# Performance work log

Hardware: AMD Instinct MI355X
Metric: run time of the kernel (lower is better)

Reference implementation:

```python
import jax, jax.numpy as jnp
import numpy as np

N = 100000   # nodes
E = 800000   # edges
F_IN = 16
H = 64       # hidden_dim
L = 4        # num_layers
CD = 8       # contrastive_dim
BN_EPS = 1e-5


def setup_inputs() -> dict:
    key = jax.random.key(0)
    ks = jax.random.split(key, 20)
    s = 0.05
    return {
        "x": jax.random.normal(ks[0], (N, F_IN), jnp.float32),
        "edge_index": jax.random.randint(ks[1], (2, E), 0, N, jnp.int64),
        "batch": jnp.zeros((N,), jnp.int64),
        "enc_w1": jax.random.normal(ks[2], (F_IN, H), jnp.float32) * s,
        "enc_b1": jnp.zeros((H,), jnp.float32),
        "enc_w2": jax.random.normal(ks[3], (H, H), jnp.float32) * s,
        "enc_b2": jnp.zeros((H,), jnp.float32),
        "conv_w": jax.random.normal(ks[4], (L, 2 * H, H), jnp.float32) * s,
        "conv_b": jnp.zeros((L, H), jnp.float32),
        "bn_gamma": jnp.ones((L, H), jnp.float32),
        "bn_beta": jnp.zeros((L, H), jnp.float32),
        "out_w1": jax.random.normal(ks[5], (H, 64), jnp.float32) * s,
        "out_b1": jnp.zeros((64,), jnp.float32),
        "out_w2": jax.random.normal(ks[6], (64, 32), jnp.float32) * s,
        "out_b2": jnp.zeros((32,), jnp.float32),
        "out_w3": jax.random.normal(ks[7], (32, CD), jnp.float32) * s,
        "out_b3": jnp.zeros((CD,), jnp.float32),
    }


def _forward(x, edge_index, enc_w1, enc_b1, enc_w2, enc_b2,
             conv_w, conv_b, bn_gamma, bn_beta,
             out_w1, out_b1, out_w2, out_b2, out_w3, out_b3):
    row, col = edge_index[0], edge_index[1]
    # lc_encode: Linear+ELU, Linear+ELU
    h = jax.nn.elu(x @ enc_w1 + enc_b1)
    feats = jax.nn.elu(h @ enc_w2 + enc_b2)  # (N, H)

    ones = jnp.ones((E, 1), feats.dtype)
    counts = jnp.clip(jax.ops.segment_sum(ones, row, num_segments=N), 1.0)  # (N,1)
    bn_scale = 1.0 / jnp.sqrt(1.0 + BN_EPS)  # eval-mode BN: running_mean=0, running_var=1

    for i in range(L):
        xc = feats[row]               # gather centers (E, H)
        xn = feats[col]               # gather neighbors (E, H)
        ef = jnp.concatenate([xc, xn - xc], axis=-1)      # (E, 2H)
        e = jax.nn.elu(ef @ conv_w[i] + conv_b[i])        # Linear + ELU
        e = (e * bn_scale) * bn_gamma[i] + bn_beta[i]     # BatchNorm (eval); Dropout is identity
        agg = jax.ops.segment_sum(e, row, num_segments=N) / counts
        feats = agg + feats  # residual in Net.forward

    # output head (Dropout identity in eval)
    o = jax.nn.elu(feats @ out_w1 + out_b1)
    o = jax.nn.elu(o @ out_w2 + out_b2)
    return o @ out_w3 + out_b3  # (N, CD)


def reference(x, edge_index, batch, enc_w1, enc_b1, enc_w2, enc_b2,
              conv_w, conv_b, bn_gamma, bn_beta,
              out_w1, out_b1, out_w2, out_b2, out_w3, out_b3):
    out = _forward(x, edge_index, enc_w1, enc_b1, enc_w2, enc_b2,
                   conv_w, conv_b, bn_gamma, bn_beta,
                   out_w1, out_b1, out_w2, out_b2, out_w3, out_b3)
    return (out, batch)
```

## Files before the change

### kernel.cpp

```cpp
#include <hip/hip_runtime.h>

#define NN 100000
#define NE 800000
#define FIN 16
#define H 64
#define NL 4
#define CDIM 8
#define NT 1563
#define NABF 1563
#define NGB 6250
#define NGF 12500
#define ROWS_PER_OWN 12500
#define ECHUNK 2048
#define NCHUNK ((NE + ECHUNK - 1) / ECHUNK)
#define NSC (NCHUNK * 8)
#define CAP 32
#define HOT 8
#define SPILL (CAP - HOT)

typedef __attribute__((ext_vector_type(8))) short bf16x8;
typedef __attribute__((ext_vector_type(4))) float f32x4;

__device__ __forceinline__ float elu(float x) { return x > 0.f ? x : __expf(x) - 1.f; }
__device__ __forceinline__ float4 elu4(float4 v) {
    return make_float4(elu(v.x), elu(v.y), elu(v.z), elu(v.w));
}

__device__ __forceinline__ unsigned short f2bf(float x) {
    union { float f; unsigned int u; } v; v.f = x;
    unsigned int r = v.u + 0x7fffu + ((v.u >> 16) & 1u);
    return (unsigned short)(r >> 16);
}
__device__ __forceinline__ float u2f(unsigned int u) {
    union { unsigned int u; float f; } v; v.u = u;
    return v.f;
}

__global__ __launch_bounds__(256) void k_enc(const float* __restrict__ x,
                                             const float* __restrict__ w1,
                                             const float* __restrict__ b1,
                                             const float* __restrict__ w2,
                                             const float* __restrict__ b2,
                                             float* __restrict__ feats,
                                             int* __restrict__ cnt,
                                             const float* __restrict__ convw,
                                             unsigned short* __restrict__ WT) {
    int tid = threadIdx.x;
    if (blockIdx.x >= NT) {
        int t = (blockIdx.x - NT) * 256 + tid;
        int i = t >> 11;
        int rem = t & 2047;
        int j = rem >> 4;
        int kg = rem & 15;
        const float* W = convw + (size_t)i * 2 * H * H;
        float v[4];
#pragma unroll
        for (int q = 0; q < 4; q++) {
            int k = kg * 4 + q;
            if (j < 64) v[q] = W[k * 64 + j] - W[(64 + k) * 64 + j];
            else        v[q] = W[(64 + k) * 64 + (j - 64)];
        }
        ushort4 p;
        p.x = f2bf(v[0]); p.y = f2bf(v[1]); p.z = f2bf(v[2]); p.w = f2bf(v[3]);
        *(ushort4*)&WT[(size_t)i * 8192 + j * 64 + kg * 4] = p;
        return;
    }
    __shared__ __align__(16) float xs[64 * 16];
    __shared__ __align__(16) float w1s[16 * 64];
    __shared__ __align__(16) float ws[64 * 64];
    __shared__ __align__(16) float fs[64 * 68];
    int base = blockIdx.x * 64;
    {
        int gid = blockIdx.x * 256 + tid;
        if (gid < NN) cnt[gid] = 0;
    }
    {
        size_t ei = (size_t)base * FIN + tid * 4;
        size_t emax = (size_t)NN * FIN - 4;
        if (ei > emax) ei = emax;
        *(float4*)&xs[tid * 4] = *(const float4*)&x[ei];
    }
    ((float4*)w1s)[tid] = ((const float4*)w1)[tid];
#pragma unroll
    for (int r = 0; r < 4; r++) ((float4*)ws)[tid + 256 * r] = ((const float4*)w2)[tid + 256 * r];
    __syncthreads();

    int wave = tid >> 6, j = tid & 63;
    float bb1 = b1[j];
    for (int i = 0; i < 16; i++) {
        int nl = i * 4 + wave;
        float acc = bb1;
#pragma unroll
        for (int k = 0; k < FIN; k++) acc += xs[nl * FIN + k] * w1s[k * 64 + j];
        fs[nl * 68 + j] = elu(acc);
    }
    __syncthreads();

    int cg = tid & 15, ng = tid >> 4;
    int c0 = cg * 4;
    float4 bb = ((const float4*)b2)[cg];
    float4 acc[4];
    acc[0] = bb; acc[1] = bb; acc[2] = bb; acc[3] = bb;
#pragma unroll 2
    for (int kq = 0; kq < 16; kq++) {
        int k0 = kq * 4;
        float4 w0 = *(const float4*)&ws[(k0 + 0) * 64 + c0];
        float4 w1v = *(const float4*)&ws[(k0 + 1) * 64 + c0];
        float4 w2v = *(const float4*)&ws[(k0 + 2) * 64 + c0];
        float4 w3v = *(const float4*)&ws[(k0 + 3) * 64 + c0];
#pragma unroll
        for (int m = 0; m < 4; m++) {
            float4 f = *(const float4*)&fs[(ng * 4 + m) * 68 + k0];
            acc[m].x += f.x * w0.x + f.y * w1v.x + f.z * w2v.x + f.w * w3v.x;
            acc[m].y += f.x * w0.y + f.y * w1v.y + f.z * w2v.y + f.w * w3v.y;
            acc[m].z += f.x * w0.z + f.y * w1v.z + f.z * w2v.z + f.w * w3v.z;
            acc[m].w += f.x * w0.w + f.y * w1v.w + f.z * w2v.w + f.w * w3v.w;
        }
    }
#pragma unroll
    for (int m = 0; m < 4; m++) {
        int n = base + ng * 4 + m;
        if (n < NN) *(float4*)&feats[(size_t)n * 64 + c0] = elu4(acc[m]);
    }
}

__global__ __launch_bounds__(256, 8) void k_scab(const int* __restrict__ row,
                                                 const int* __restrict__ col,
                                                 int* cnt, int* __restrict__ hot,
                                                 int* __restrict__ spill,
                                                 const float* __restrict__ feats,
                                                 const unsigned short* __restrict__ WT,
                                                 const float* __restrict__ convb,
                                                 unsigned short* __restrict__ Am,
                                                 unsigned short* __restrict__ Bm) {
    int tid = threadIdx.x;
    if (blockIdx.x < NSC) {
        int owner = blockIdx.x & 7;
        int chunk = blockIdx.x >> 3;
        int lo = owner * ROWS_PER_OWN, hi = lo + ROWS_PER_OWN;
        int base = chunk * ECHUNK;
        int end = base + ECHUNK; if (end > NE) end = NE;
        for (int e = base + tid; e < end; e += 256) {
            int r = row[e];
            if (r >= lo && r < hi) {
                int p = atomicAdd(&cnt[r], 1);
                if (p < HOT) hot[(size_t)r * HOT + p] = col[e];
                else if (p < CAP) spill[(size_t)r * SPILL + (p - HOT)] = col[e];
            }
        }
        return;
    }
    int bid = blockIdx.x - NSC;
    int wave = tid >> 6, lane = tid & 63;
    int lr = lane & 15, lk = lane >> 4;
    int nb = bid * 64 + wave * 16;
    int n = nb + lr;
    int nc = n < NN ? n : NN - 1;

    bf16x8 ff0, ff1;
    {
        float4 f0 = *(const float4*)&feats[(size_t)nc * 64 + lk * 8];
        float4 f1 = *(const float4*)&feats[(size_t)nc * 64 + lk * 8 + 4];
        float4 f2 = *(const float4*)&feats[(size_t)nc * 64 + 32 + lk * 8];
        float4 f3 = *(const float4*)&feats[(size_t)nc * 64 + 32 + lk * 8 + 4];
        ff0[0] = (short)f2bf(f0.x); ff0[1] = (short)f2bf(f0.y);
        ff0[2] = (short)f2bf(f0.z); ff0[3] = (short)f2bf(f0.w);
        ff0[4] = (short)f2bf(f1.x); ff0[5] = (short)f2bf(f1.y);
        ff0[6] = (short)f2bf(f1.z); ff0[7] = (short)f2bf(f1.w);
        ff1[0] = (short)f2bf(f2.x); ff1[1] = (short)f2bf(f2.y);
        ff1[2] = (short)f2bf(f2.z); ff1[3] = (short)f2bf(f2.w);
        ff1[4] = (short)f2bf(f3.x); ff1[5] = (short)f2bf(f3.y);
        ff1[6] = (short)f2bf(f3.z); ff1[7] = (short)f2bf(f3.w);
    }
#pragma unroll 1
    for (int ct = 0; ct < 8; ct++) {
        bf16x8 w0 = *(const bf16x8*)&WT[(ct * 16 + lr) * 64 + lk * 8];
        bf16x8 w1 = *(const bf16x8*)&WT[(ct * 16 + lr) * 64 + 32 + lk * 8];
        f32x4 acc;
        if (ct < 4) {
            float4 bq = *(const float4*)&convb[ct * 16 + lk * 4];
            acc[0] = bq.x; acc[1] = bq.y; acc[2] = bq.z; acc[3] = bq.w;
        } else {
            acc = (f32x4)(0.0f);
        }
        acc = __builtin_amdgcn_mfma_f32_16x16x32_bf16(w0, ff0, acc, 0, 0, 0);
        acc = __builtin_amdgcn_mfma_f32_16x16x32_bf16(w1, ff1, acc, 0, 0, 0);
        if (n < NN) {
            unsigned short* dst = (ct < 4) ? Am : Bm;
            int wc = (ct & 3) * 16 + lk * 4;
            ushort4 p;
            p.x = f2bf(acc[0]); p.y = f2bf(acc[1]);
            p.z = f2bf(acc[2]); p.w = f2bf(acc[3]);
            *(ushort4*)&dst[(size_t)n * 64 + wc] = p;
        }
    }
}

__global__ __launch_bounds__(256) void k_gab(const unsigned short* __restrict__ Brd,
                                             unsigned short* __restrict__ Am,
                                             unsigned short* __restrict__ Bwr,
                                             const int* __restrict__ cnt,
                                             const int* __restrict__ hot,
                                             const int* __restrict__ spill,
                                             const float* __restrict__ gamma,
                                             const float* __restrict__ beta,
                                             float* __restrict__ feats,
                                             const unsigned short* __restrict__ WT,
                                             const float* __restrict__ convb) {
    __shared__ __align__(16) unsigned short nlds[16 * 72];
    int tid = threadIdx.x;
    int wave = tid >> 6, lane = tid & 63;
    int half = lane >> 5, l = lane & 31;
    int g = l >> 3;
    int cq = l & 7, c0 = cq * 8;
    int nb16 = blockIdx.x * 16;

    const float bs = 0.99999500003749968750f;
    float4 gm0 = *(const float4*)&gamma[c0];
    float4 gm1 = *(const float4*)&gamma[c0 + 4];
    float4 bt0 = *(const float4*)&beta[c0];
    float4 bt1 = *(const float4*)&beta[c0 + 4];

#pragma unroll
    for (int t = 0; t < 2; t++) {
        int j = t * 8 + wave * 2 + half;
        int n = nb16 + j;
        int deg = cnt[n];
        if (deg > CAP) deg = CAP;
        int mycol = (l < HOT) ? hot[(size_t)n * HOT + l]
                              : spill[(size_t)n * SPILL + (l - HOT)];
        uint4 rawA = *(const uint4*)&Am[(size_t)n * H + c0];
        float4 a0 = make_float4(u2f(rawA.x << 16), u2f(rawA.x & 0xffff0000u),
                                u2f(rawA.y << 16), u2f(rawA.y & 0xffff0000u));
        float4 a1 = make_float4(u2f(rawA.z << 16), u2f(rawA.z & 0xffff0000u),
                                u2f(rawA.w << 16), u2f(rawA.w & 0xffff0000u));
        float4 f0, f1;
        if (g == 0) {
            f0 = *(const float4*)&feats[(size_t)n * H + c0];
            f1 = *(const float4*)&feats[(size_t)n * H + c0 + 4];
        }
        float4 acc0 = make_float4(0.f, 0.f, 0.f, 0.f);
        float4 acc1 = make_float4(0.f, 0.f, 0.f, 0.f);
        for (int p0 = 0; p0 < deg; p0 += 4) {
            int p = p0 + g;
            bool valid = p < deg;
            int pc = valid ? p : (deg - 1);
            int c = __shfl(mycol, (half << 5) + pc);
            uint4 raw = *(const uint4*)&Brd[(size_t)c * H + c0];
            float4 b0 = make_float4(u2f(raw.x << 16), u2f(raw.x & 0xffff0000u),
                                    u2f(raw.y << 16), u2f(raw.y & 0xffff0000u));
            float4 b1 = make_float4(u2f(raw.z << 16), u2f(raw.z & 0xffff0000u),
                                    u2f(raw.w << 16), u2f(raw.w & 0xffff0000u));
            float4 v0 = elu4(make_float4(a0.x + b0.x, a0.y + b0.y, a0.z + b0.z, a0.w + b0.w));
            float4 v1 = elu4(make_float4(a1.x + b1.x, a1.y + b1.y, a1.z + b1.z, a1.w + b1.w));
            if (valid) {
                acc0.x += v0.x; acc0.y += v0.y; acc0.z += v0.z; acc0.w += v0.w;
                acc1.x += v1.x; acc1.y += v1.y; acc1.z += v1.z; acc1.w += v1.w;
            }
        }
#pragma unroll
        for (int d = 8; d < 32; d <<= 1) {
            acc0.x += __shfl_xor(acc0.x, d); acc0.y += __shfl_xor(acc0.y, d);
            acc0.z += __shfl_xor(acc0.z, d); acc0.w += __shfl_xor(acc0.w, d);
            acc1.x += __shfl_xor(acc1.x, d); acc1.y += __shfl_xor(acc1.y, d);
            acc1.z += __shfl_xor(acc1.z, d); acc1.w += __shfl_xor(acc1.w, d);
        }
        if (g == 0) {
            if (deg > 0) {
                float inv = bs / (float)deg;
                f0.x += acc0.x * gm0.x * inv + bt0.x;
                f0.y += acc0.y * gm0.y * inv + bt0.y;
                f0.z += acc0.z * gm0.z * inv + bt0.z;
                f0.w += acc0.w * gm0.w * inv + bt0.w;
                f1.x += acc1.x * gm1.x * inv + bt1.x;
                f1.y += acc1.y * gm1.y * inv + bt1.y;
                f1.z += acc1.z * gm1.z * inv + bt1.z;
                f1.w += acc1.w * gm1.w * inv + bt1.w;
                *(float4*)&feats[(size_t)n * H + c0] = f0;
                *(float4*)&feats[(size_t)n * H + c0 + 4] = f1;
            }
            ushort4 pa, pb;
            pa.x = f2bf(f0.x); pa.y = f2bf(f0.y); pa.z = f2bf(f0.z); pa.w = f2bf(f0.w);
            pb.x = f2bf(f1.x); pb.y = f2bf(f1.y); pb.z = f2bf(f1.z); pb.w = f2bf(f1.w);
            *(ushort4*)&nlds[j * 72 + cq * 8] = pa;
            *(ushort4*)&nlds[j * 72 + cq * 8 + 4] = pb;
        }
    }
    __syncthreads();

    {
        int lr = lane & 15, lk = lane >> 4;
        bf16x8 ff[2];
#pragma unroll
        for (int kt = 0; kt < 2; kt++)
            ff[kt] = *(const bf16x8*)&nlds[lr * 72 + kt * 32 + lk * 8];
#pragma unroll
        for (int ctl = 0; ctl < 2; ctl++) {
            int ct = wave * 2 + ctl;
            bf16x8 w0 = *(const bf16x8*)&WT[(ct * 16 + lr) * 64 + lk * 8];
            bf16x8 w1 = *(const bf16x8*)&WT[(ct * 16 + lr) * 64 + 32 + lk * 8];
            f32x4 acc;
            if (ct < 4) {
                float4 bq = *(const float4*)&convb[ct * 16 + lk * 4];
                acc[0] = bq.x; acc[1] = bq.y; acc[2] = bq.z; acc[3] = bq.w;
            } else {
                acc = (f32x4)(0.0f);
            }
            acc = __builtin_amdgcn_mfma_f32_16x16x32_bf16(w0, ff[0], acc, 0, 0, 0);
            acc = __builtin_amdgcn_mfma_f32_16x16x32_bf16(w1, ff[1], acc, 0, 0, 0);
            int n = nb16 + lr;
            unsigned short* dst = (ct < 4) ? Am : Bwr;
            int wc = (ct & 3) * 16 + lk * 4;
            ushort4 p;
            p.x = f2bf(acc[0]); p.y = f2bf(acc[1]);
            p.z = f2bf(acc[2]); p.w = f2bf(acc[3]);
            *(ushort4*)&dst[(size_t)n * 64 + wc] = p;
        }
    }
}

__global__ __launch_bounds__(256) void k_gather(const unsigned short* __restrict__ Am,
                                                const unsigned short* __restrict__ Bm,
                                                const int* __restrict__ cnt,
                                                const int* __restrict__ hot,
                                                const int* __restrict__ spill,
                                                const float* __restrict__ gamma,
                                                const float* __restrict__ beta,
                                                float* __restrict__ feats) {
    int tid = threadIdx.x;
    int wave = tid >> 6, lane = tid & 63;
    int half = lane >> 5, l = lane & 31;
    int n = blockIdx.x * 8 + wave * 2 + half;
    int g = l >> 3;
    int cq = l & 7, c0 = cq * 8;
    int deg = cnt[n];
    if (deg > CAP) deg = CAP;
    int mycol = (l < HOT) ? hot[(size_t)n * HOT + l]
                          : spill[(size_t)n * SPILL + (l - HOT)];
    uint4 rawA = *(const uint4*)&Am[(size_t)n * H + c0];
    float4 a0 = make_float4(u2f(rawA.x << 16), u2f(rawA.x & 0xffff0000u),
                            u2f(rawA.y << 16), u2f(rawA.y & 0xffff0000u));
    float4 a1 = make_float4(u2f(rawA.z << 16), u2f(rawA.z & 0xffff0000u),
                            u2f(rawA.w << 16), u2f(rawA.w & 0xffff0000u));
    float4 f0, f1;
    if (g == 0) {
        f0 = *(const float4*)&feats[(size_t)n * H + c0];
        f1 = *(const float4*)&feats[(size_t)n * H + c0 + 4];
    }
    float4 acc0 = make_float4(0.f, 0.f, 0.f, 0.f);
    float4 acc1 = make_float4(0.f, 0.f, 0.f, 0.f);
    for (int p0 = 0; p0 < deg; p0 += 4) {
        int p = p0 + g;
        bool valid = p < deg;
        int pc = valid ? p : (deg - 1);
        int c = __shfl(mycol, (half << 5) + pc);
        uint4 raw = *(const uint4*)&Bm[(size_t)c * H + c0];
        float4 b0 = make_float4(u2f(raw.x << 16), u2f(raw.x & 0xffff0000u),
                                u2f(raw.y << 16), u2f(raw.y & 0xffff0000u));
        float4 b1 = make_float4(u2f(raw.z << 16), u2f(raw.z & 0xffff0000u),
                                u2f(raw.w << 16), u2f(raw.w & 0xffff0000u));
        float4 v0 = elu4(make_float4(a0.x + b0.x, a0.y + b0.y, a0.z + b0.z, a0.w + b0.w));
        float4 v1 = elu4(make_float4(a1.x + b1.x, a1.y + b1.y, a1.z + b1.z, a1.w + b1.w));
        if (valid) {
            acc0.x += v0.x; acc0.y += v0.y; acc0.z += v0.z; acc0.w += v0.w;
            acc1.x += v1.x; acc1.y += v1.y; acc1.z += v1.z; acc1.w += v1.w;
        }
    }
#pragma unroll
    for (int d = 8; d < 32; d <<= 1) {
        acc0.x += __shfl_xor(acc0.x, d); acc0.y += __shfl_xor(acc0.y, d);
        acc0.z += __shfl_xor(acc0.z, d); acc0.w += __shfl_xor(acc0.w, d);
        acc1.x += __shfl_xor(acc1.x, d); acc1.y += __shfl_xor(acc1.y, d);
        acc1.z += __shfl_xor(acc1.z, d); acc1.w += __shfl_xor(acc1.w, d);
    }
    if (g == 0 && deg > 0) {
        const float bs = 0.99999500003749968750f;
        float inv = bs / (float)deg;
        float4 gm0 = *(const float4*)&gamma[c0];
        float4 gm1 = *(const float4*)&gamma[c0 + 4];
        float4 bt0 = *(const float4*)&beta[c0];
        float4 bt1 = *(const float4*)&beta[c0 + 4];
        f0.x += acc0.x * gm0.x * inv + bt0.x;
        f0.y += acc0.y * gm0.y * inv + bt0.y;
        f0.z += acc0.z * gm0.z * inv + bt0.z;
        f0.w += acc0.w * gm0.w * inv + bt0.w;
        f1.x += acc1.x * gm1.x * inv + bt1.x;
        f1.y += acc1.y * gm1.y * inv + bt1.y;
        f1.z += acc1.z * gm1.z * inv + bt1.z;
        f1.w += acc1.w * gm1.w * inv + bt1.w;
        *(float4*)&feats[(size_t)n * H + c0] = f0;
        *(float4*)&feats[(size_t)n * H + c0 + 4] = f1;
    }
}

__global__ __launch_bounds__(256) void k_head(const float* __restrict__ feats,
                                              const float* __restrict__ w1,
                                              const float* __restrict__ b1,
                                              const float* __restrict__ w2,
                                              const float* __restrict__ b2,
                                              const float* __restrict__ w3,
                                              const float* __restrict__ b3,
                                              const int* __restrict__ batch,
                                              float* __restrict__ out,
                                              float* __restrict__ out2) {
    __shared__ __align__(16) float fs[64 * 68];
    __shared__ __align__(16) float w1s[64 * 64];
    __shared__ __align__(16) float o1s[64 * 68];
    __shared__ __align__(16) float w2s[64 * 32];
    __shared__ __align__(16) float w3s[32 * 8];
    int tid = threadIdx.x;
    int base = blockIdx.x * 64;
#pragma unroll
    for (int r = 0; r < 4; r++) {
        int idx = tid + 256 * r;
        ((float4*)w1s)[idx] = ((const float4*)w1)[idx];
        int rw = idx >> 4, cc = idx & 15;
        int n = base + rw; if (n >= NN) n = NN - 1;
        *(float4*)&fs[rw * 68 + cc * 4] = *(const float4*)&feats[(size_t)n * 64 + cc * 4];
    }
    ((float4*)w2s)[tid] = ((const float4*)w2)[tid];
    ((float4*)w2s)[tid + 256] = ((const float4*)w2)[tid + 256];
    if (tid < 64) ((float4*)w3s)[tid] = ((const float4*)w3)[tid];
    if (tid < 64) {
        int n = base + tid;
        if (n < NN) out2[n] = (float)batch[n];
    }
    __syncthreads();

    int cg = tid & 15, ng = tid >> 4;
    int c0 = cg * 4;
    {
        float4 bb = ((const float4*)b1)[cg];
        float4 acc[4];
        acc[0] = bb; acc[1] = bb; acc[2] = bb; acc[3] = bb;
#pragma unroll 2
        for (int kq = 0; kq < 16; kq++) {
            int k0 = kq * 4;
            float4 w0 = *(const float4*)&w1s[(k0 + 0) * 64 + c0];
            float4 w1v = *(const float4*)&w1s[(k0 + 1) * 64 + c0];
            float4 w2v = *(const float4*)&w1s[(k0 + 2) * 64 + c0];
            float4 w3v = *(const float4*)&w1s[(k0 + 3) * 64 + c0];
#pragma unroll
            for (int m = 0; m < 4; m++) {
                float4 f = *(const float4*)&fs[(ng * 4 + m) * 68 + k0];
                acc[m].x += f.x * w0.x + f.y * w1v.x + f.z * w2v.x + f.w * w3v.x;
                acc[m].y += f.x * w0.y + f.y * w1v.y + f.z * w2v.y + f.w * w3v.y;
                acc[m].z += f.x * w0.z + f.y * w1v.z + f.z * w2v.z + f.w * w3v.z;
                acc[m].w += f.x * w0.w + f.y * w1v.w + f.z * w2v.w + f.w * w3v.w;
            }
        }
        __syncthreads();
#pragma unroll
        for (int m = 0; m < 4; m++)
            *(float4*)&o1s[(ng * 4 + m) * 68 + c0] = elu4(acc[m]);
    }
    __syncthreads();

    float* o2s = fs;
    {
        int cg2 = tid & 7, ng2 = tid >> 3;
        int c20 = cg2 * 4;
        float4 bb = ((const float4*)b2)[cg2];
        float4 acc[2];
        acc[0] = bb; acc[1] = bb;
#pragma unroll 2
        for (int kq = 0; kq < 16; kq++) {
            int k0 = kq * 4;
            float4 w0 = *(const float4*)&w2s[(k0 + 0) * 32 + c20];
            float4 w1v = *(const float4*)&w2s[(k0 + 1) * 32 + c20];
            float4 w2v = *(const float4*)&w2s[(k0 + 2) * 32 + c20];
            float4 w3v = *(const float4*)&w2s[(k0 + 3) * 32 + c20];
#pragma unroll
            for (int m = 0; m < 2; m++) {
                float4 f = *(const float4*)&o1s[(ng2 * 2 + m) * 68 + k0];
                acc[m].x += f.x * w0.x + f.y * w1v.x + f.z * w2v.x + f.w * w3v.x;
                acc[m].y += f.x * w0.y + f.y * w1v.y + f.z * w2v.y + f.w * w3v.y;
                acc[m].z += f.x * w0.z + f.y * w1v.z + f.z * w2v.z + f.w * w3v.z;
                acc[m].w += f.x * w0.w + f.y * w1v.w + f.z * w2v.w + f.w * w3v.w;
            }
        }
#pragma unroll
        for (int m = 0; m < 2; m++)
            *(float4*)&o2s[(ng2 * 2 + m) * 40 + c20] = elu4(acc[m]);
    }
    __syncthreads();

    if (tid < 128) {
        int n3 = tid >> 1, c30 = (tid & 1) * 4;
        float4 acc = ((const float4*)b3)[tid & 1];
#pragma unroll 2
        for (int kq = 0; kq < 8; kq++) {
            int k0 = kq * 4;
            float4 w0 = *(const float4*)&w3s[(k0 + 0) * 8 + c30];
            float4 w1v = *(const float4*)&w3s[(k0 + 1) * 8 + c30];
            float4 w2v = *(const float4*)&w3s[(k0 + 2) * 8 + c30];
            float4 w3v = *(const float4*)&w3s[(k0 + 3) * 8 + c30];
            float4 f = *(const float4*)&o2s[n3 * 40 + k0];
            acc.x += f.x * w0.x + f.y * w1v.x + f.z * w2v.x + f.w * w3v.x;
            acc.y += f.x * w0.y + f.y * w1v.y + f.z * w2v.y + f.w * w3v.y;
            acc.z += f.x * w0.z + f.y * w1v.z + f.z * w2v.z + f.w * w3v.z;
            acc.w += f.x * w0.w + f.y * w1v.w + f.z * w2v.w + f.w * w3v.w;
        }
        int n = base + n3;
        if (n < NN) *(float4*)&out[(size_t)n * 8 + c30] = acc;
    }
}

extern "C" void kernel_launch(void* const* d_in, const int* in_sizes, int n_in,
                              void* d_out, int out_size, void* d_ws, size_t ws_size,
                              hipStream_t stream) {
    const float* x = (const float*)d_in[0];
    const int* edge_index = (const int*)d_in[1];
    const int* batch = (const int*)d_in[2];
    const float* enc_w1 = (const float*)d_in[3];
    const float* enc_b1 = (const float*)d_in[4];
    const float* enc_w2 = (const float*)d_in[5];
    const float* enc_b2 = (const float*)d_in[6];
    const float* conv_w = (const float*)d_in[7];
    const float* conv_b = (const float*)d_in[8];
    const float* bn_gamma = (const float*)d_in[9];
    const float* bn_beta = (const float*)d_in[10];
    const float* out_w1 = (const float*)d_in[11];
    const float* out_b1 = (const float*)d_in[12];
    const float* out_w2 = (const float*)d_in[13];
    const float* out_b2 = (const float*)d_in[14];
    const float* out_w3 = (const float*)d_in[15];
    const float* out_b3 = (const float*)d_in[16];

    const int* row = edge_index;
    const int* col = edge_index + NE;

    float* feats = (float*)d_ws;
    unsigned short* Abuf = (unsigned short*)(feats + (size_t)NN * H);
    unsigned short* Bbuf0 = Abuf + (size_t)NN * H;
    unsigned short* Bbuf1 = Bbuf0 + (size_t)NN * H;
    int* cnt = (int*)(Bbuf1 + (size_t)NN * H);
    int* hot = cnt + NN;
    int* spill = hot + (size_t)NN * HOT;
    unsigned short* WT = (unsigned short*)(spill + (size_t)NN * SPILL);

    float* out = (float*)d_out;

    k_enc<<<NT + 32, 256, 0, stream>>>(x, enc_w1, enc_b1, enc_w2, enc_b2, feats, cnt,
                                       conv_w, WT);
    k_scab<<<NSC + NABF, 256, 0, stream>>>(row, col, cnt, hot, spill,
                                           feats, WT, conv_b, Abuf, Bbuf0);

    unsigned short* Brd = Bbuf0;
    unsigned short* Bwr = Bbuf1;
    for (int i = 0; i < NL - 1; i++) {
        k_gab<<<NGB, 256, 0, stream>>>(Brd, Abuf, Bwr, cnt, hot, spill,
                                       bn_gamma + (size_t)i * H, bn_beta + (size_t)i * H,
                                       feats, WT + (size_t)(i + 1) * 8192,
                                       conv_b + (size_t)(i + 1) * H);
        unsigned short* tmp = Brd; Brd = Bwr; Bwr = tmp;
    }
    k_gather<<<NGF, 256, 0, stream>>>(Abuf, Brd, cnt, hot, spill,
                                      bn_gamma + (size_t)(NL - 1) * H,
                                      bn_beta + (size_t)(NL - 1) * H, feats);

    k_head<<<NT, 256, 0, stream>>>(feats, out_w1, out_b1, out_w2, out_b2,
                                   out_w3, out_b3, batch, out,
                                   out + (size_t)NN * CDIM);
}
```

Before: 371.2 us.

## Fuse layer-0 edge-weight MFMA into encoder kernel and split scatter out

The encoder kernel now converts its output tile to bf16 in shared memory, rebuilds the layer-0 transformed weight matrix in LDS per block, and runs the MFMA producing the A/B projections directly. This removes the re-read of feats in a separate kernel. The edge scatter becomes its own kernel using int4 row loads. The cost is larger LDS use per block and redundant per-block weight conversion from global fp32 conv weights.

```diff
diff --git a/kernel.cpp b/kernel.cpp
--- a/kernel.cpp
+++ b/kernel.cpp
@@ -7,7 +7,6 @@
 #define NL 4
 #define CDIM 8
 #define NT 1563
-#define NABF 1563
 #define NGB 6250
 #define NGF 12500
 #define ROWS_PER_OWN 12500
@@ -36,15 +35,47 @@
     return v.f;
 }
 
-__global__ __launch_bounds__(256) void k_enc(const float* __restrict__ x,
-                                             const float* __restrict__ w1,
-                                             const float* __restrict__ b1,
-                                             const float* __restrict__ w2,
-                                             const float* __restrict__ b2,
-                                             float* __restrict__ feats,
-                                             int* __restrict__ cnt,
-                                             const float* __restrict__ convw,
-                                             unsigned short* __restrict__ WT) {
+__global__ __launch_bounds__(256) void k_scatter(const int* __restrict__ row,
+                                                 const int* __restrict__ col,
+                                                 int* cnt, int* __restrict__ hot,
+                                                 int* __restrict__ spill) {
+    int owner = blockIdx.x & 7;
+    int chunk = blockIdx.x >> 3;
+    int lo = owner * ROWS_PER_OWN, hi = lo + ROWS_PER_OWN;
+    int base = chunk * ECHUNK;
+    int end = base + ECHUNK; if (end > NE) end = NE;
+    int tid = threadIdx.x;
+#pragma unroll
+    for (int q = 0; q < 2; q++) {
+        int e0 = base + (q * 256 + tid) * 4;
+        if (e0 < end) {
+            int4 r4 = *(const int4*)&row[e0];
+            int rr0 = r4.x, rr1 = r4.y, rr2 = r4.z, rr3 = r4.w;
+#pragma unroll
+            for (int u = 0; u < 4; u++) {
+                int r = (u == 0) ? rr0 : (u == 1) ? rr1 : (u == 2) ? rr2 : rr3;
+                if (r >= lo && r < hi) {
+                    int p = atomicAdd(&cnt[r], 1);
+                    if (p < HOT) hot[(size_t)r * HOT + p] = col[e0 + u];
+                    else if (p < CAP) spill[(size_t)r * SPILL + (p - HOT)] = col[e0 + u];
+                }
+            }
+        }
+    }
+}
+
+__global__ __launch_bounds__(256) void k_encab(const float* __restrict__ x,
+                                               const float* __restrict__ w1,
+                                               const float* __restrict__ b1,
+                                               const float* __restrict__ w2,
+                                               const float* __restrict__ b2,
+                                               float* __restrict__ feats,
+                                               int* __restrict__ cnt,
+                                               const float* __restrict__ convw,
+                                               unsigned short* __restrict__ WT,
+                                               const float* __restrict__ convb,
+                                               unsigned short* __restrict__ Am,
+                                               unsigned short* __restrict__ Bm) {
     int tid = threadIdx.x;
     if (blockIdx.x >= NT) {
         int t = (blockIdx.x - NT) * 256 + tid;
@@ -65,10 +96,14 @@
         *(ushort4*)&WT[(size_t)i * 8192 + j * 64 + kg * 4] = p;
         return;
     }
-    __shared__ __align__(16) float xs[64 * 16];
-    __shared__ __align__(16) float w1s[16 * 64];
-    __shared__ __align__(16) float ws[64 * 64];
-    __shared__ __align__(16) float fs[64 * 68];
+    __shared__ __align__(16) char smem[41984];
+    float* xs  = (float*)smem;
+    float* w1s = xs + 1024;
+    float* ws  = w1s + 1024;
+    float* fs  = ws + 4096;
+    unsigned short* ntile = (unsigned short*)smem;
+    unsigned short* wlds  = (unsigned short*)(smem + 9216);
+
     int base = blockIdx.x * 64;
     {
         int gid = blockIdx.x * 256 + tid;
@@ -85,113 +120,95 @@
     for (int r = 0; r < 4; r++) ((float4*)ws)[tid + 256 * r] = ((const float4*)w2)[tid + 256 * r];
     __syncthreads();
 
-    int wave = tid >> 6, j = tid & 63;
-    float bb1 = b1[j];
-    for (int i = 0; i < 16; i++) {
-        int nl = i * 4 + wave;
-        float acc = bb1;
-#pragma unroll
-        for (int k = 0; k < FIN; k++) acc += xs[nl * FIN + k] * w1s[k * 64 + j];
-        fs[nl * 68 + j] = elu(acc);
+    int wave = tid >> 6, lane = tid & 63;
+    {
+        int j = lane;
+        float bb1 = b1[j];
+        for (int i = 0; i < 16; i++) {
+            int nl = i * 4 + wave;
+            float acc = bb1;
+#pragma unroll
+            for (int k = 0; k < FIN; k++) acc += xs[nl * FIN + k] * w1s[k * 64 + j];
+            fs[nl * 68 + j] = elu(acc);
+        }
     }
     __syncthreads();
 
     int cg = tid & 15, ng = tid >> 4;
     int c0 = cg * 4;
-    float4 bb = ((const float4*)b2)[cg];
     float4 acc[4];
-    acc[0] = bb; acc[1] = bb; acc[2] = bb; acc[3] = bb;
+    {
+        float4 bb = ((const float4*)b2)[cg];
+        acc[0] = bb; acc[1] = bb; acc[2] = bb; acc[3] = bb;
 #pragma unroll 2
-    for (int kq = 0; kq < 16; kq++) {
-        int k0 = kq * 4;
-        float4 w0 = *(const float4*)&ws[(k0 + 0) * 64 + c0];
-        float4 w1v = *(const float4*)&ws[(k0 + 1) * 64 + c0];
-        float4 w2v = *(const float4*)&ws[(k0 + 2) * 64 + c0];
-        float4 w3v = *(const float4*)&ws[(k0 + 3) * 64 + c0];
-#pragma unroll
-        for (int m = 0; m < 4; m++) {
-            float4 f = *(const float4*)&fs[(ng * 4 + m) * 68 + k0];
-            acc[m].x += f.x * w0.x + f.y * w1v.x + f.z * w2v.x + f.w * w3v.x;
-            acc[m].y += f.x * w0.y + f.y * w1v.y + f.z * w2v.y + f.w * w3v.y;
-            acc[m].z += f.x * w0.z + f.y * w1v.z + f.z * w2v.z + f.w * w3v.z;
-            acc[m].w += f.x * w0.w + f.y * w1v.w + f.z * w2v.w + f.w * w3v.w;
-        }
-    }
+        for (int kq = 0; kq < 16; kq++) {
+            int k0 = kq * 4;
+            float4 w0 = *(const float4*)&ws[(k0 + 0) * 64 + c0];
+            float4 w1v = *(const float4*)&ws[(k0 + 1) * 64 + c0];
+            float4 w2v = *(const float4*)&ws[(k0 + 2) * 64 + c0];
+            float4 w3v = *(const float4*)&ws[(k0 + 3) * 64 + c0];
+#pragma unroll
+            for (int m = 0; m < 4; m++) {
+                float4 f = *(const float4*)&fs[(ng * 4 + m) * 68 + k0];
+                acc[m].x += f.x * w0.x + f.y * w1v.x + f.z * w2v.x + f.w * w3v.x;
+                acc[m].y += f.x * w0.y + f.y * w1v.y + f.z * w2v.y + f.w * w3v.y;
+                acc[m].z += f.x * w0.z + f.y * w1v.z + f.z * w2v.z + f.w * w3v.z;
+                acc[m].w += f.x * w0.w + f.y * w1v.w + f.z * w2v.w + f.w * w3v.w;
+            }
+        }
+    }
+    __syncthreads();
+
 #pragma unroll
     for (int m = 0; m < 4; m++) {
-        int n = base + ng * 4 + m;
-        if (n < NN) *(float4*)&feats[(size_t)n * 64 + c0] = elu4(acc[m]);
-    }
-}
-
-__global__ __launch_bounds__(256, 8) void k_scab(const int* __restrict__ row,
-                                                 const int* __restrict__ col,
-                                                 int* cnt, int* __restrict__ hot,
-                                                 int* __restrict__ spill,
-                                                 const float* __restrict__ feats,
-                                                 const unsigned short* __restrict__ WT,
-                                                 const float* __restrict__ convb,
-                                                 unsigned short* __restrict__ Am,
-                                                 unsigned short* __restrict__ Bm) {
-    int tid = threadIdx.x;
-    if (blockIdx.x < NSC) {
-        int owner = blockIdx.x & 7;
-        int chunk = blockIdx.x >> 3;
-        int lo = owner * ROWS_PER_OWN, hi = lo + ROWS_PER_OWN;
-        int base = chunk * ECHUNK;
-        int end = base + ECHUNK; if (end > NE) end = NE;
-        for (int e = base + tid; e < end; e += 256) {
-            int r = row[e];
-            if (r >= lo && r < hi) {
-                int p = atomicAdd(&cnt[r], 1);
-                if (p < HOT) hot[(size_t)r * HOT + p] = col[e];
-                else if (p < CAP) spill[(size_t)r * SPILL + (p - HOT)] = col[e];
-            }
-        }
-        return;
-    }
-    int bid = blockIdx.x - NSC;
-    int wave = tid >> 6, lane = tid & 63;
-    int lr = lane & 15, lk = lane >> 4;
-    int nb = bid * 64 + wave * 16;
-    int n = nb + lr;
-    int nc = n < NN ? n : NN - 1;
-
-    bf16x8 ff0, ff1;
-    {
-        float4 f0 = *(const float4*)&feats[(size_t)nc * 64 + lk * 8];
-        float4 f1 = *(const float4*)&feats[(size_t)nc * 64 + lk * 8 + 4];
-        float4 f2 = *(const float4*)&feats[(size_t)nc * 64 + 32 + lk * 8];
-        float4 f3 = *(const float4*)&feats[(size_t)nc * 64 + 32 + lk * 8 + 4];
-        ff0[0] = (short)f2bf(f0.x); ff0[1] = (short)f2bf(f0.y);
-        ff0[2] = (short)f2bf(f0.z); ff0[3] = (short)f2bf(f0.w);
-        ff0[4] = (short)f2bf(f1.x); ff0[5] = (short)f2bf(f1.y);
-        ff0[6] = (short)f2bf(f1.z); ff0[7] = (short)f2bf(f1.w);
-        ff1[0] = (short)f2bf(f2.x); ff1[1] = (short)f2bf(f2.y);
-        ff1[2] = (short)f2bf(f2.z); ff1[3] = (short)f2bf(f2.w);
-        ff1[4] = (short)f2bf(f3.x); ff1[5] = (short)f2bf(f3.y);
-        ff1[6] = (short)f2bf(f3.z); ff1[7] = (short)f2bf(f3.w);
-    }
+        float4 e = elu4(acc[m]);
+        int nl = ng * 4 + m;
+        int n = base + nl;
+        if (n < NN) *(float4*)&feats[(size_t)n * 64 + c0] = e;
+        ushort4 p;
+        p.x = f2bf(e.x); p.y = f2bf(e.y); p.z = f2bf(e.z); p.w = f2bf(e.w);
+        *(ushort4*)&ntile[nl * 72 + c0] = p;
+    }
+    {
+        int k = tid & 63;
+        int jb = (tid >> 6) * 32;
+#pragma unroll 4
+        for (int jj = 0; jj < 32; jj++) {
+            int j = jb + jj;
+            float v;
+            if (j < 64) v = convw[k * 64 + j] - convw[(64 + k) * 64 + j];
+            else        v = convw[(64 + k) * 64 + (j - 64)];
+            wlds[j * 72 + k] = f2bf(v);
+        }
+    }
+    __syncthreads();
+
+    {
+        int lr = lane & 15, lk = lane >> 4;
+        int n = base + wave * 16 + lr;
+        bf16x8 ff0 = *(const bf16x8*)&ntile[(wave * 16 + lr) * 72 + lk * 8];
+        bf16x8 ff1 = *(const bf16x8*)&ntile[(wave * 16 + lr) * 72 + 32 + lk * 8];
 #pragma unroll 1
-    for (int ct = 0; ct < 8; ct++) {
-        bf16x8 w0 = *(const bf16x8*)&WT[(ct * 16 + lr) * 64 + lk * 8];
-        bf16x8 w1 = *(const bf16x8*)&WT[(ct * 16 + lr) * 64 + 32 + lk * 8];
-        f32x4 acc;
-        if (ct < 4) {
-            float4 bq = *(const float4*)&convb[ct * 16 + lk * 4];
-            acc[0] = bq.x; acc[1] = bq.y; acc[2] = bq.z; acc[3] = bq.w;
-        } else {
-            acc = (f32x4)(0.0f);
-        }
-        acc = __builtin_amdgcn_mfma_f32_16x16x32_bf16(w0, ff0, acc, 0, 0, 0);
-        acc = __builtin_amdgcn_mfma_f32_16x16x32_bf16(w1, ff1, acc, 0, 0, 0);
-        if (n < NN) {
-            unsigned short* dst = (ct < 4) ? Am : Bm;
-            int wc = (ct & 3) * 16 + lk * 4;
-            ushort4 p;
-            p.x = f2bf(acc[0]); p.y = f2bf(acc[1]);
-            p.z = f2bf(acc[2]); p.w = f2bf(acc[3]);
-            *(ushort4*)&dst[(size_t)n * 64 + wc] = p;
+        for (int ct = 0; ct < 8; ct++) {
+            bf16x8 w0 = *(const bf16x8*)&wlds[(ct * 16 + lr) * 72 + lk * 8];
+            bf16x8 w1f = *(const bf16x8*)&wlds[(ct * 16 + lr) * 72 + 32 + lk * 8];
+            f32x4 a;
+            if (ct < 4) {
+                float4 bq = *(const float4*)&convb[ct * 16 + lk * 4];
+                a[0] = bq.x; a[1] = bq.y; a[2] = bq.z; a[3] = bq.w;
+            } else {
+                a = (f32x4)(0.0f);
+            }
+            a = __builtin_amdgcn_mfma_f32_16x16x32_bf16(w0, ff0, a, 0, 0, 0);
+            a = __builtin_amdgcn_mfma_f32_16x16x32_bf16(w1f, ff1, a, 0, 0, 0);
+            if (n < NN) {
+                unsigned short* dst = (ct < 4) ? Am : Bm;
+                int wc = (ct & 3) * 16 + lk * 4;
+                ushort4 p;
+                p.x = f2bf(a[0]); p.y = f2bf(a[1]);
+                p.z = f2bf(a[2]); p.w = f2bf(a[3]);
+                *(ushort4*)&dst[(size_t)n * 64 + wc] = p;
+            }
         }
     }
 }
@@ -541,10 +558,9 @@
 
     float* out = (float*)d_out;
 
-    k_enc<<<NT + 32, 256, 0, stream>>>(x, enc_w1, enc_b1, enc_w2, enc_b2, feats, cnt,
-                                       conv_w, WT);
-    k_scab<<<NSC + NABF, 256, 0, stream>>>(row, col, cnt, hot, spill,
-                                           feats, WT, conv_b, Abuf, Bbuf0);
+    k_encab<<<NT + 32, 256, 0, stream>>>(x, enc_w1, enc_b1, enc_w2, enc_b2, feats, cnt,
+                                         conv_w, WT, conv_b, Abuf, Bbuf0);
+    k_scatter<<<NSC, 256, 0, stream>>>(row, col, cnt, hot, spill);
 
     unsigned short* Brd = Bbuf0;
     unsigned short* Bwr = Bbuf1;
```

Result: slower. 387.6 us (+4.4%).
